# Performance work log

Measured on AMD Instinct MI355X. Metric: run time of the kernel, lower is better.

## Reference

```python
import jax, jax.numpy as jnp
import numpy as np
import math

B, S, D_IN, D_OUT = 2, 2048, 2048, 2048
N_HEADS, N_KV = 32, 8
HEAD_DIM = D_OUT // N_HEADS  # 64
GROUP = N_HEADS // N_KV      # 4


def _rope_tables(seq_len, head_dim, base=10000.0):
    inv_freq = 1.0 / (base ** (jnp.arange(0, head_dim, 2, dtype=jnp.float32) / head_dim))
    angles = jnp.arange(seq_len, dtype=jnp.float32)[:, None] * inv_freq[None, :]  # [S, hd/2]
    angles = jnp.concatenate([angles, angles], axis=-1)  # [S, hd]
    return jnp.cos(angles), jnp.sin(angles)


def setup_inputs() -> dict:
    key = jax.random.key(0)
    kx, kq, kk, kv, ko = jax.random.split(key, 5)
    x = jax.random.normal(kx, (B, S, D_IN), dtype=jnp.float32)
    # causal mask: True where attention is disallowed (j > i)
    mask = jnp.triu(jnp.ones((S, S), dtype=bool), k=1)
    cos, sin = _rope_tables(S, HEAD_DIM)
    scale = 0.02
    Wq = jax.random.normal(kq, (D_IN, D_OUT), dtype=jnp.float32) * scale
    Wk = jax.random.normal(kk, (D_IN, N_KV * HEAD_DIM), dtype=jnp.float32) * scale
    Wv = jax.random.normal(kv, (D_IN, N_KV * HEAD_DIM), dtype=jnp.float32) * scale
    Wo = jax.random.normal(ko, (D_OUT, D_OUT), dtype=jnp.float32) * scale
    return {"x": x, "mask": mask, "cos": cos, "sin": sin,
            "Wq": Wq, "Wk": Wk, "Wv": Wv, "Wo": Wo}


def _apply_rope(t, cos, sin):
    # t: [B, H, S, hd]; cos/sin: [S, hd]
    hd = t.shape[-1]
    t1, t2 = t[..., : hd // 2], t[..., hd // 2:]
    rotated = jnp.concatenate([-t2, t1], axis=-1)
    return t * cos[None, None] + rotated * sin[None, None]


def reference(x, mask, cos, sin, Wq, Wk, Wv, Wo):
    b, s, _ = x.shape
    q = (x @ Wq).reshape(b, s, N_HEADS, HEAD_DIM).transpose(0, 2, 1, 3)  # [B,H,S,hd]
    k = (x @ Wk).reshape(b, s, N_KV, HEAD_DIM).transpose(0, 2, 1, 3)    # [B,G,S,hd]
    v = (x @ Wv).reshape(b, s, N_KV, HEAD_DIM).transpose(0, 2, 1, 3)
    q = _apply_rope(q, cos, sin)
    k = _apply_rope(k, cos, sin)
    # repeat_interleave KV heads to match query heads
    k = jnp.repeat(k, GROUP, axis=1)  # [B,H,S,hd]
    v = jnp.repeat(v, GROUP, axis=1)
    scores = jnp.einsum('bhqd,bhkd->bhqk', q, k)
    scores = jnp.where(mask[None, None], -1e9, scores)
    weights = jax.nn.softmax(scores / math.sqrt(HEAD_DIM), axis=-1)
    ctx = jnp.einsum('bhqk,bhkd->bhqd', weights, v)
    ctx = ctx.transpose(0, 2, 1, 3).reshape(b, s, D_OUT)
    return ctx @ Wo
```

## Files before the change

### kernel.cpp

```cpp
#include <hip/hip_runtime.h>
#include <hip/hip_bf16.h>

using bf16 = __bf16;
using bf16x8 = __attribute__((ext_vector_type(8))) __bf16;
using bf16x4 = __attribute__((ext_vector_type(4))) __bf16;
using f32x4  = __attribute__((ext_vector_type(4))) float;
using f32x16 = __attribute__((ext_vector_type(16))) float;

typedef const void __attribute__((address_space(1)))* gas_p;
typedef void __attribute__((address_space(3)))* las_p;

#define GLD16(g, l) __builtin_amdgcn_global_load_lds((gas_p)(const void*)(g), (las_p)(void*)(l), 16, 0, 0)

__device__ __forceinline__ bf16x8 lds_ld8(const void* p) {
  union { uint4 u; bf16x8 v; } c;
  c.u = *(const uint4*)p;
  return c.v;
}
__device__ __forceinline__ bf16x8 g_ld8(const bf16* p) {
  union { uint4 u; bf16x8 v; } c;
  c.u = *(const uint4*)p;
  return c.v;
}
__device__ __forceinline__ float fexp2(float x) {
  float r; asm("v_exp_f32 %0, %1" : "=v"(r) : "v"(x)); return r;
}
__device__ __forceinline__ unsigned cvtpk(float lo, float hi) {
  unsigned r; asm("v_cvt_pk_bf16_f32 %0, %1, %2" : "=v"(r) : "v"(lo), "v"(hi)); return r;
}

__global__ void k_convert(const float* __restrict__ in, bf16* __restrict__ out, int n4) {
  int i = blockIdx.x * blockDim.x + threadIdx.x;
  if (i >= n4) return;
  float4 f = ((const float4*)in)[i];
  bf16x4 o;
  o[0] = (bf16)f.x; o[1] = (bf16)f.y; o[2] = (bf16)f.z; o[3] = (bf16)f.w;
  ((bf16x4*)out)[i] = o;
}

__global__ void k_transp_all(const float* __restrict__ Wq, const float* __restrict__ Wk,
                             const float* __restrict__ Wv, const float* __restrict__ Wo,
                             bf16* __restrict__ wqkv, bf16* __restrict__ wo_t) {
  __shared__ float tile[64][65];
  const int id = blockIdx.x;
  const float* W; bf16* dst; int N, rowOff, bx, by;
  if (id < 1024)      { W = Wq; dst = wqkv; N = 2048; rowOff = 0;    bx = id & 31;          by = id >> 5; }
  else if (id < 1280) { int u = id - 1024; W = Wk; dst = wqkv; N = 512; rowOff = 2048; bx = u & 7; by = u >> 3; }
  else if (id < 1536) { int u = id - 1280; W = Wv; dst = wqkv; N = 512; rowOff = 2560; bx = u & 7; by = u >> 3; }
  else                { int u = id - 1536; W = Wo; dst = wo_t; N = 2048; rowOff = 0;   bx = u & 31; by = u >> 5; }
  const int n0 = bx * 64, k0 = by * 64;
  const int t = threadIdx.x;
#pragma unroll
  for (int i = 0; i < 16; ++i) {
    int idx = t + i * 256; int r = idx >> 6, c = idx & 63;
    tile[r][c] = W[(size_t)(k0 + r) * N + n0 + c];
  }
  __syncthreads();
#pragma unroll
  for (int i = 0; i < 16; ++i) {
    int idx = t + i * 256; int r = idx >> 6, c = idx & 63;
    dst[(size_t)(rowOff + n0 + r) * 2048 + k0 + c] = (bf16)tile[c][r];
  }
}

__device__ __forceinline__ void gemm_main(const bf16* __restrict__ A, const bf16* __restrict__ Bt,
                                          int brow, int bcol, int tid, f32x4 (&acc)[4][4],
                                          char* ldsA, char* ldsB) {
  const int lane = tid & 63;
  const int l15 = lane & 15, l4 = lane >> 4;
  const int wid = tid >> 6, wr = wid >> 1, wc = wid & 1;
  const int srow = tid >> 3;
  const int xseg = (tid & 7) ^ (srow & 7);
  const bf16* ga = A  + (size_t)(brow + srow) * 2048 + xseg * 8;
  const bf16* gb = Bt + (size_t)(bcol + srow) * 2048 + xseg * 8;
  char* la = ldsA + tid * 16;
  char* lb = ldsB + tid * 16;

  for (int k0 = 0; k0 < 2048; k0 += 64) {
    __syncthreads();
#pragma unroll
    for (int i = 0; i < 4; ++i) {
      GLD16(ga + k0 + (size_t)(32 * i) * 2048, la + i * 4096);
      GLD16(gb + k0 + (size_t)(32 * i) * 2048, lb + i * 4096);
    }
    __syncthreads();
#pragma unroll
    for (int kk = 0; kk < 2; ++kk) {
      bf16x8 af[4], bfr[4];
#pragma unroll
      for (int m = 0; m < 4; ++m) {
        const int row = wr * 64 + m * 16 + l15;
        af[m] = lds_ld8(ldsA + row * 128 + ((kk * 64 + l4 * 16) ^ ((row & 7) << 4)));
      }
#pragma unroll
      for (int n = 0; n < 4; ++n) {
        const int row = wc * 64 + n * 16 + l15;
        bfr[n] = lds_ld8(ldsB + row * 128 + ((kk * 64 + l4 * 16) ^ ((row & 7) << 4)));
      }
#pragma unroll
      for (int m = 0; m < 4; ++m)
#pragma unroll
        for (int n = 0; n < 4; ++n)
          acc[m][n] = __builtin_amdgcn_mfma_f32_16x16x32_bf16(af[m], bfr[n], acc[m][n], 0, 0, 0);
    }
  }
}

__global__ __launch_bounds__(256) void k_gemm_qkv(const bf16* __restrict__ A, const bf16* __restrict__ Bt,
    const float* __restrict__ cosT, const float* __restrict__ sinT,
    bf16* __restrict__ Qb, bf16* __restrict__ Kb, bf16* __restrict__ Vt) {
  __shared__ __align__(16) char ldsA[16384];
  __shared__ __align__(16) char ldsB[16384];
  const int tid = threadIdx.x;
  const int p = (int)blockIdx.x, r8 = p & 7, q8 = p >> 3;
  const int by = r8 * 3 + q8 % 3, bx = q8 / 3;
  const int brow = bx * 128, bcol = by * 128;
  f32x4 zero = {0.f, 0.f, 0.f, 0.f};
  f32x4 acc[4][4];
#pragma unroll
  for (int m = 0; m < 4; ++m)
#pragma unroll
    for (int n = 0; n < 4; ++n) acc[m][n] = zero;

  gemm_main(A, Bt, brow, bcol, tid, acc, ldsA, ldsB);

  const int lane = tid & 63, l15 = lane & 15, l4 = lane >> 4;
  const int wid = tid >> 6, wr = wid >> 1, wc = wid & 1;
  const int base64 = bcol + wc * 64;
  const int rbase  = brow + wr * 64;

  if (base64 < 2048) {
    const int h = base64 >> 6;
#pragma unroll
    for (int m = 0; m < 4; ++m)
#pragma unroll
      for (int r = 0; r < 4; ++r) {
        const int row = rbase + m * 16 + l4 * 4 + r;
        const int b = row >> 11, s = row & 2047;
        float o[4];
#pragma unroll
        for (int n = 0; n < 4; ++n) {
          const int d = n * 16 + l15;
          const float cv = cosT[s * 64 + d], sv = sinT[s * 64 + d];
          const float t = acc[m][n][r], pp = acc[m][n ^ 2][r];
          o[n] = (t * cv + ((n < 2) ? -pp : pp) * sv) * 0.18033688f;
        }
        bf16* dst = Qb + ((size_t)((b * 32 + h) * 2048 + s)) * 64;
#pragma unroll
        for (int n = 0; n < 4; ++n) dst[n * 16 + l15] = (bf16)o[n];
      }
  } else if (base64 < 2560) {
    const int h = (base64 - 2048) >> 6;
#pragma unroll
    for (int m = 0; m < 4; ++m)
#pragma unroll
      for (int r = 0; r < 4; ++r) {
        const int row = rbase + m * 16 + l4 * 4 + r;
        const int b = row >> 11, s = row & 2047;
        float o[4];
#pragma unroll
        for (int n = 0; n < 4; ++n) {
          const int d = n * 16 + l15;
          const float cv = cosT[s * 64 + d], sv = sinT[s * 64 + d];
          const float t = acc[m][n][r], pp = acc[m][n ^ 2][r];
          o[n] = t * cv + ((n < 2) ? -pp : pp) * sv;
        }
        bf16* dst = Kb + ((size_t)((b * 8 + h) * 2048 + s)) * 64;
#pragma unroll
        for (int n = 0; n < 4; ++n) dst[n * 16 + l15] = (bf16)o[n];
      }
  } else {
    const int h = (base64 - 2560) >> 6;
#pragma unroll
    for (int m = 0; m < 4; ++m)
#pragma unroll
      for (int r = 0; r < 4; ++r) {
        const int row = rbase + m * 16 + l4 * 4 + r;
        const int b = row >> 11, s = row & 2047;
        const int ps = (s & ~12) | ((s & 4) << 1) | ((s & 8) >> 1);
#pragma unroll
        for (int n = 0; n < 4; ++n) {
          const int d = n * 16 + l15;
          Vt[((size_t)((b * 8 + h) * 64 + d)) * 2048 + ps] = (bf16)acc[m][n][r];
        }
      }
  }
}

__global__ __launch_bounds__(256) void k_attn(const bf16* __restrict__ Qb, const bf16* __restrict__ Kb,
                                              const bf16* __restrict__ Vtp, bf16* __restrict__ ctx) {
  __shared__ __align__(16) char kvb[2][16384];
  const int tid = threadIdx.x, lane = tid & 63, w = tid >> 6;
  const int l31 = lane & 31, hi = lane >> 5;
  const int p = (int)blockIdx.x;
  const int y = (p & 7) * 8 + ((p >> 3) & 7);
  const int j = p >> 6;
  const int c = (int)((0xD95126AEC84037BFULL >> (4 * j)) & 15);
  const int b = y >> 5, h = y & 31, hk = h >> 2;
  const int q0 = c * 128 + w * 32;
  const int nf = (q0 + 31) >> 6;
  const int nt = 2 * c + 2;

  const int srow = tid >> 3, sseg = tid & 7;
  const bf16* kS = Kb  + ((size_t)((b * 8 + hk) * 2048)) * 64;
  const bf16* vS = Vtp + ((size_t)((b * 8 + hk) * 64)) * 2048;

  const bf16* qbase = Qb + ((size_t)((b * 32 + h) * 2048 + q0 + l31)) * 64 + hi * 8;
  bf16x8 bq[4];
#pragma unroll
  for (int dc = 0; dc < 4; ++dc) bq[dc] = g_ld8(qbase + dc * 16);

  const f32x16 z16 = {0,0,0,0,0,0,0,0,0,0,0,0,0,0,0,0};
  f32x16 o[2] = {z16, z16};
  float m = -3.0e38f, lsum = 0.f;
  const int sz = (l31 & 7) << 4;
  const int wsz = (srow & 7) << 4;

  uint4 st[4];
  auto stage_load = [&](int kv0) {
#pragma unroll
    for (int r4 = 0; r4 < 4; ++r4) {
      const int row = srow + (r4 & 1) * 32;
      const bf16* g = (r4 < 2) ? (kS + (size_t)(kv0 + row) * 64 + sseg * 8)
                               : (vS + (size_t)row * 2048 + kv0 + sseg * 8);
      st[r4] = *(const uint4*)g;
    }
  };
  auto stage_write = [&](char* buf) {
#pragma unroll
    for (int r4 = 0; r4 < 4; ++r4)
      *(uint4*)(buf + (srow + r4 * 32) * 128 + ((sseg * 16) ^ wsz)) = st[r4];
  };

  stage_load(0);
  stage_write(kvb[0]);
  __syncthreads();

  for (int kt = 0; kt < nt; ++kt) {
    char* cur = kvb[kt & 1];
    if (kt + 1 < nt) stage_load((kt + 1) * 64);
    if (kt <= nf) {
      const int kv0 = kt * 64;
      f32x16 sc[2];
      __builtin_amdgcn_s_setprio(1);
#pragma unroll
      for (int kvh = 0; kvh < 2; ++kvh) {
        const int row = kvh * 32 + l31;
        bf16x8 a0 = lds_ld8(cur + row * 128 + ((hi * 16) ^ sz));
        sc[kvh] = __builtin_amdgcn_mfma_f32_32x32x16_bf16(a0, bq[0], z16, 0, 0, 0);
#pragma unroll
        for (int dc = 1; dc < 4; ++dc) {
          bf16x8 ad = lds_ld8(cur + row * 128 + ((dc * 32 + hi * 16) ^ sz));
          sc[kvh] = __builtin_amdgcn_mfma_f32_32x32x16_bf16(ad, bq[dc], sc[kvh], 0, 0, 0);
        }
      }
      __builtin_amdgcn_s_setprio(0);
      if (kt == nf) {
        const int q = q0 + l31;
#pragma unroll
        for (int kvh = 0; kvh < 2; ++kvh)
#pragma unroll
          for (int r = 0; r < 16; ++r) {
            const int kv = kv0 + kvh * 32 + (r & 3) + 8 * (r >> 2) + 4 * hi;
            if (kv > q) sc[kvh][r] = -3.0e30f;
          }
      }
      float t[16];
#pragma unroll
      for (int i = 0; i < 16; ++i) t[i] = fmaxf(sc[0][i], sc[1][i]);
#pragma unroll
      for (int stp = 8; stp >= 1; stp >>= 1)
#pragma unroll
        for (int i = 0; i < stp; ++i) t[i] = fmaxf(t[i], t[i + stp]);
      float mx = fmaxf(t[0], __shfl_xor(t[0], 32));
      if (!__all(mx <= m + 11.5f)) {
        const float mn = fmaxf(m, mx);
        const float corr = fexp2(m - mn);
        m = mn;
        lsum *= corr;
#pragma unroll
        for (int r = 0; r < 16; ++r) { o[0][r] *= corr; o[1][r] *= corr; }
      }
#pragma unroll
      for (int kvh = 0; kvh < 2; ++kvh)
#pragma unroll
        for (int r = 0; r < 16; ++r) sc[kvh][r] = fexp2(sc[kvh][r] - m);
#pragma unroll
      for (int kvh = 0; kvh < 2; ++kvh)
#pragma unroll
        for (int s = 0; s < 2; ++s) {
          union { unsigned u[4]; bf16x8 v; } f;
#pragma unroll
          for (int tt = 0; tt < 4; ++tt)
            f.u[tt] = cvtpk(sc[kvh][s * 8 + 2 * tt], sc[kvh][s * 8 + 2 * tt + 1]);
          const int cc = kvh * 2 + s;
          __builtin_amdgcn_s_setprio(1);
#pragma unroll
          for (int dh = 0; dh < 2; ++dh) {
            const int row = 64 + dh * 32 + l31;
            bf16x8 av = lds_ld8(cur + row * 128 + ((cc * 32 + hi * 16) ^ sz));
            o[dh] = __builtin_amdgcn_mfma_f32_32x32x16_bf16(av, f.v, o[dh], 0, 0, 0);
          }
          __builtin_amdgcn_s_setprio(0);
        }
      float u[16];
#pragma unroll
      for (int i = 0; i < 16; ++i) u[i] = sc[0][i] + sc[1][i];
#pragma unroll
      for (int stp = 8; stp >= 1; stp >>= 1)
#pragma unroll
        for (int i = 0; i < stp; ++i) u[i] += u[i + stp];
      lsum += u[0];
    }
    if (kt + 1 < nt) stage_write(kvb[(kt + 1) & 1]);
    __syncthreads();
  }

  float ll = lsum + __shfl_xor(lsum, 32);
  const float inv = 1.0f / ll;
  char* tb = kvb[0] + w * 4096;
#pragma unroll
  for (int dh = 0; dh < 2; ++dh)
#pragma unroll
    for (int r = 0; r < 16; r += 2) {
      const unsigned wdv = cvtpk(o[dh][r] * inv, o[dh][r + 1] * inv);
      const int d = dh * 32 + (r & 3) + 8 * (r >> 2) + 4 * hi;
      *(unsigned*)(tb + l31 * 128 + ((d * 2) ^ sz)) = wdv;
    }
#pragma unroll
  for (int jj = 0; jj < 4; ++jj) {
    const int off = hi * 16 + jj * 32;
    uint4 val = *(const uint4*)(tb + l31 * 128 + (off ^ sz));
    *(uint4*)(ctx + ((size_t)(b * 2048 + q0 + l31)) * 2048 + h * 64 + off / 2) = val;
  }
}

__global__ __launch_bounds__(256) void k_gemm_out(const bf16* __restrict__ A, const bf16* __restrict__ Bt,
                                                  float* __restrict__ out) {
  __shared__ __align__(16) char ldsA[16384];
  __shared__ __align__(16) char ldsB[16384];
  const int tid = threadIdx.x;
  const int p = (int)blockIdx.x, r8 = p & 7, q8 = p >> 3;
  const int by = r8 * 2 + (q8 & 1), bx = q8 >> 1;
  const int brow = bx * 128, bcol = by * 128;
  f32x4 zero = {0.f, 0.f, 0.f, 0.f};
  f32x4 acc[4][4];
#pragma unroll
  for (int m = 0; m < 4; ++m)
#pragma unroll
    for (int n = 0; n < 4; ++n) acc[m][n] = zero;

  gemm_main(A, Bt, brow, bcol, tid, acc, ldsA, ldsB);

  const int lane = tid & 63, l15 = lane & 15, l4 = lane >> 4;
  const int wid = tid >> 6, wr = wid >> 1, wc = wid & 1;
#pragma unroll
  for (int m = 0; m < 4; ++m)
#pragma unroll
    for (int r = 0; r < 4; ++r) {
      const int row = brow + wr * 64 + m * 16 + l4 * 4 + r;
      float* dst = out + (size_t)row * 2048 + bcol + wc * 64;
#pragma unroll
      for (int n = 0; n < 4; ++n) dst[n * 16 + l15] = acc[m][n][r];
    }
}

extern "C" void kernel_launch(void* const* d_in, const int* in_sizes, int n_in,
                              void* d_out, int out_size, void* d_ws, size_t ws_size,
                              hipStream_t stream) {
  (void)in_sizes; (void)n_in; (void)out_size;
  if (ws_size < (size_t)79691776) return;
  const float* x    = (const float*)d_in[0];
  const float* cosT = (const float*)d_in[2];
  const float* sinT = (const float*)d_in[3];
  const float* Wq   = (const float*)d_in[4];
  const float* Wk   = (const float*)d_in[5];
  const float* Wv   = (const float*)d_in[6];
  const float* Wo   = (const float*)d_in[7];
  char* ws = (char*)d_ws;
  bf16* xb   = (bf16*)(ws + 0);
  bf16* wqkv = (bf16*)(ws + 16777216);
  bf16* wo_t = (bf16*)(ws + 29360128);
  bf16* Qb   = (bf16*)(ws + 37748736);
  bf16* Kb   = (bf16*)(ws + 54525952);
  bf16* Vt   = (bf16*)(ws + 58720256);
  bf16* ctxb = (bf16*)(ws + 62914560);
  float* out = (float*)d_out;

  k_convert<<<8192, 256, 0, stream>>>(x, xb, 2097152);
  k_transp_all<<<2560, 256, 0, stream>>>(Wq, Wk, Wv, Wo, wqkv, wo_t);
  k_gemm_qkv<<<768, 256, 0, stream>>>(xb, wqkv, cosT, sinT, Qb, Kb, Vt);
  k_attn<<<1024, 256, 0, stream>>>(Qb, Kb, Vt, ctxb);
  k_gemm_out<<<512, 256, 0, stream>>>(ctxb, wo_t, out);
}
```

Baseline: 233.9 us.

## Pair complementary causal query tiles per attention block for balanced work

Each attention block now handles two query tiles, c=15-j and c=j, processed back to back in one fused loop of 34 KV tiles. The grid is halved from 1024 to 512 blocks. This balances the triangular causal workload so every block does the same amount of work, removing tail imbalance and the static ordering table. A separate transpose buffer is added for the mid-loop epilogue, which raises LDS use and may lower occupancy. The work is now serialized within fewer blocks.

New measurement: 211.4 us. -9.6%, faster.

```diff
diff --git a/kernel.cpp b/kernel.cpp
--- a/kernel.cpp
+++ b/kernel.cpp
@@ -190,31 +190,37 @@
 __global__ __launch_bounds__(256) void k_attn(const bf16* __restrict__ Qb, const bf16* __restrict__ Kb,
                                               const bf16* __restrict__ Vtp, bf16* __restrict__ ctx) {
   __shared__ __align__(16) char kvb[2][16384];
+  __shared__ __align__(16) char tbuf[4][4096];
   const int tid = threadIdx.x, lane = tid & 63, w = tid >> 6;
   const int l31 = lane & 31, hi = lane >> 5;
   const int p = (int)blockIdx.x;
   const int y = (p & 7) * 8 + ((p >> 3) & 7);
   const int j = p >> 6;
-  const int c = (int)((0xD95126AEC84037BFULL >> (4 * j)) & 15);
   const int b = y >> 5, h = y & 31, hk = h >> 2;
-  const int q0 = c * 128 + w * 32;
-  const int nf = (q0 + 31) >> 6;
-  const int nt = 2 * c + 2;
+  const int ntA = 2 * (15 - j) + 2;
+  const int NT = 34;
 
   const int srow = tid >> 3, sseg = tid & 7;
   const bf16* kS = Kb  + ((size_t)((b * 8 + hk) * 2048)) * 64;
   const bf16* vS = Vtp + ((size_t)((b * 8 + hk) * 64)) * 2048;
-
-  const bf16* qbase = Qb + ((size_t)((b * 32 + h) * 2048 + q0 + l31)) * 64 + hi * 8;
-  bf16x8 bq[4];
-#pragma unroll
-  for (int dc = 0; dc < 4; ++dc) bq[dc] = g_ld8(qbase + dc * 16);
-
-  const f32x16 z16 = {0,0,0,0,0,0,0,0,0,0,0,0,0,0,0,0};
-  f32x16 o[2] = {z16, z16};
-  float m = -3.0e38f, lsum = 0.f;
   const int sz = (l31 & 7) << 4;
   const int wsz = (srow & 7) << 4;
+
+  const f32x16 z16 = {0,0,0,0,0,0,0,0,0,0,0,0,0,0,0,0};
+  f32x16 o[2];
+  float m, lsum;
+  bf16x8 bq[4];
+  int c = 15 - j;
+  int q0 = c * 128 + w * 32;
+  int nf = (q0 + 31) >> 6;
+
+  auto load_q = [&]() {
+    const bf16* qbase = Qb + ((size_t)((b * 32 + h) * 2048 + q0 + l31)) * 64 + hi * 8;
+#pragma unroll
+    for (int dc = 0; dc < 4; ++dc) bq[dc] = g_ld8(qbase + dc * 16);
+  };
+  load_q();
+  o[0] = z16; o[1] = z16; m = -3.0e38f; lsum = 0.f;
 
   uint4 st[4];
   auto stage_load = [&](int kv0) {
@@ -232,13 +238,38 @@
       *(uint4*)(buf + (srow + r4 * 32) * 128 + ((sseg * 16) ^ wsz)) = st[r4];
   };
 
+  auto epilogue = [&]() {
+    float ll = lsum + __shfl_xor(lsum, 32);
+    const float inv = 1.0f / ll;
+    char* tb = tbuf[w];
+#pragma unroll
+    for (int dh = 0; dh < 2; ++dh)
+#pragma unroll
+      for (int r = 0; r < 16; r += 2) {
+        const unsigned wdv = cvtpk(o[dh][r] * inv, o[dh][r + 1] * inv);
+        const int d = dh * 32 + (r & 3) + 8 * (r >> 2) + 4 * hi;
+        *(unsigned*)(tb + l31 * 128 + ((d * 2) ^ sz)) = wdv;
+      }
+#pragma unroll
+    for (int jj = 0; jj < 4; ++jj) {
+      const int off = hi * 16 + jj * 32;
+      uint4 val = *(const uint4*)(tb + l31 * 128 + (off ^ sz));
+      *(uint4*)(ctx + ((size_t)(b * 2048 + q0 + l31)) * 2048 + h * 64 + off / 2) = val;
+    }
+  };
+
   stage_load(0);
   stage_write(kvb[0]);
   __syncthreads();
 
-  for (int kt = 0; kt < nt; ++kt) {
-    char* cur = kvb[kt & 1];
-    if (kt + 1 < nt) stage_load((kt + 1) * 64);
+  for (int g = 0; g < NT; ++g) {
+    const int kt = (g < ntA) ? g : g - ntA;
+    char* cur = kvb[g & 1];
+    if (g + 1 < NT) {
+      const int gn = g + 1;
+      const int ktn = (gn < ntA) ? gn : gn - ntA;
+      stage_load(ktn * 64);
+    }
     if (kt <= nf) {
       const int kv0 = kt * 64;
       f32x16 sc[2];
@@ -312,27 +343,16 @@
         for (int i = 0; i < stp; ++i) u[i] += u[i + stp];
       lsum += u[0];
     }
-    if (kt + 1 < nt) stage_write(kvb[(kt + 1) & 1]);
+    if (g + 1 < NT) stage_write(kvb[(g + 1) & 1]);
     __syncthreads();
+    if (g == ntA - 1) {
+      epilogue();
+      c = j; q0 = c * 128 + w * 32; nf = (q0 + 31) >> 6;
+      load_q();
+      o[0] = z16; o[1] = z16; m = -3.0e38f; lsum = 0.f;
+    }
   }
-
-  float ll = lsum + __shfl_xor(lsum, 32);
-  const float inv = 1.0f / ll;
-  char* tb = kvb[0] + w * 4096;
-#pragma unroll
-  for (int dh = 0; dh < 2; ++dh)
-#pragma unroll
-    for (int r = 0; r < 16; r += 2) {
-      const unsigned wdv = cvtpk(o[dh][r] * inv, o[dh][r + 1] * inv);
-      const int d = dh * 32 + (r & 3) + 8 * (r >> 2) + 4 * hi;
-      *(unsigned*)(tb + l31 * 128 + ((d * 2) ^ sz)) = wdv;
-    }
-#pragma unroll
-  for (int jj = 0; jj < 4; ++jj) {
-    const int off = hi * 16 + jj * 32;
-    uint4 val = *(const uint4*)(tb + l31 * 128 + (off ^ sz));
-    *(uint4*)(ctx + ((size_t)(b * 2048 + q0 + l31)) * 2048 + h * 64 + off / 2) = val;
-  }
+  epilogue();
 }
 
 __global__ __launch_bounds__(256) void k_gemm_out(const bf16* __restrict__ A, const bf16* __restrict__ Bt,
@@ -390,6 +410,6 @@
   k_convert<<<8192, 256, 0, stream>>>(x, xb, 2097152);
   k_transp_all<<<2560, 256, 0, stream>>>(Wq, Wk, Wv, Wo, wqkv, wo_t);
   k_gemm_qkv<<<768, 256, 0, stream>>>(xb, wqkv, cosT, sinT, Qb, Kb, Vt);
-  k_attn<<<1024, 256, 0, stream>>>(Qb, Kb, Vt, ctxb);
+  k_attn<<<512, 256, 0, stream>>>(Qb, Kb, Vt, ctxb);
   k_gemm_out<<<512, 256, 0, stream>>>(ctxb, wo_t, out);
 }
```
